# Kernel tuning notes

Hardware: AMD Instinct MI355X
Metric: run time of the kernel (lower is better)

## Reference

```python
import jax, jax.numpy as jnp
import numpy as np


def _rope_tables(T, d):
    half = d // 2
    i = jnp.arange(half, dtype=jnp.float32)
    theta = 10000.0 ** (-2.0 * i / d)          # [half]
    m = jnp.arange(T, dtype=jnp.float32)[:, None]  # [T,1]
    ang = m * theta[None, :]                    # [T,half]
    return jnp.cos(ang), jnp.sin(ang)


def _rotate(v, cos, sin):
    # interleaved even/odd RoPE rotation, vectorized
    B, T, d = v.shape
    half = d // 2
    v2 = v.reshape(B, T, half, 2)
    even, odd = v2[..., 0], v2[..., 1]
    c = cos[None, :, :]
    s = sin[None, :, :]
    new_even = even * c - odd * s
    new_odd = even * s + odd * c
    return jnp.stack([new_even, new_odd], axis=-1).reshape(B, T, d)


def setup_inputs() -> dict:
    key = jax.random.key(0)
    k1, k2, k3, k4 = jax.random.split(key, 4)
    B, T, d = 4, 2048, 1024
    x = jax.random.normal(k1, (B, T, d), dtype=jnp.float32)
    scale = 0.02
    Wq = jax.random.normal(k2, (d, d), dtype=jnp.float32) * scale
    Wk = jax.random.normal(k3, (d, d), dtype=jnp.float32) * scale
    Wv = jax.random.normal(k4, (d, d), dtype=jnp.float32) * scale
    return {"x": x, "Wq": Wq, "Wk": Wk, "Wv": Wv}


def reference(x, Wq, Wk, Wv):
    B, T, d = x.shape
    cos, sin = _rope_tables(T, d)
    # torch Linear: y = x @ W.T
    Q = jnp.einsum('btd,ed->bte', x, Wq)
    K = jnp.einsum('btd,ed->bte', x, Wk)
    V = jnp.einsum('btd,ed->bte', x, Wv)
    Qr = _rotate(Q, cos, sin)
    Kr = _rotate(K, cos, sin)
    scores = jnp.einsum('bqd,bkd->bqk', Qr, Kr) / jnp.sqrt(jnp.float32(d))
    # NOTE: original uses tril with diagonal=1 (allows one future position)
    mask = jnp.tril(jnp.ones((T, T), dtype=bool), k=1)
    scores = jnp.where(mask[None, :, :], scores, -jnp.inf)
    attn = jax.nn.softmax(scores, axis=-1)
    out = jnp.einsum('bqk,bkd->bqd', attn, V)
    return out
```

## Files before the change

kernel.cpp:

```cpp
#include <hip/hip_runtime.h>


typedef float f32x4 __attribute__((ext_vector_type(4)));
typedef __bf16 bf16x8 __attribute__((ext_vector_type(8)));

#define BM 128
#define BN 128
#define BK 64

#define SP_BATCH 2473984

__device__ __forceinline__ unsigned short f2bf(float f) {
  union { float f; unsigned int u; } c; c.f = f;
  unsigned int u = c.u;
  u += 0x7fffu + ((u >> 16) & 1u);
  return (unsigned short)(u >> 16);
}
__device__ __forceinline__ float bf2f(unsigned short h) {
  union { unsigned int u; float f; } c; c.u = ((unsigned int)h) << 16;
  return c.f;
}

__device__ __forceinline__ void async16(const unsigned short* gp, unsigned short* lp) {
  __builtin_amdgcn_global_load_lds(
      (const __attribute__((address_space(1))) void*)gp,
      (__attribute__((address_space(3))) void*)lp, 16, 0, 0);
}

__global__ __launch_bounds__(256) void cvt_all(
    const float4* __restrict__ x, const float4* __restrict__ wq,
    const float4* __restrict__ wk, const float4* __restrict__ wv,
    ushort4* __restrict__ xb, ushort4* __restrict__ wb,
    float4* __restrict__ rowsums) {
  int b = blockIdx.x, t = threadIdx.x;
  if (b == 11264) {
#pragma unroll
    for (int i = 0; i < 8; ++i) rowsums[i * 256 + t] = float4{0.f, 0.f, 0.f, 0.f};
    return;
  }
  const float4* src;
  ushort4* dst;
  long i;
  if (b < 8192) { src = x; dst = xb; i = (long)b * 256 + t; }
  else if (b < 9216) { src = wq; dst = wb; i = (long)(b - 8192) * 256 + t; }
  else if (b < 10240) { src = wk; dst = wb + 262144; i = (long)(b - 9216) * 256 + t; }
  else { src = wv; dst = wb + 524288; i = (long)(b - 10240) * 256 + t; }
  float4 v = src[i];
  ushort4 o;
  o.x = f2bf(v.x); o.y = f2bf(v.y); o.z = f2bf(v.z); o.w = f2bf(v.w);
  dst[i] = o;
}

template <int IM, int JN>
__device__ __forceinline__ void gemm_body(
    const unsigned short* __restrict__ A, const unsigned short* __restrict__ B,
    unsigned short* As, unsigned short* Bs,
    int lda, int ldb, int m0, int n0, int ktiles,
    int tid, int lane, int wave, f32x4 (&acc)[IM][JN]) {
  const int wm = (wave >> 1) * (IM * 16);
  const int wn = (wave & 1) * (JN * 16);
  const int fm = lane & 15;
  const int q = lane >> 4;
  const int srow = tid >> 3;
  const int c = (tid & 7) ^ (srow & 7);
  const unsigned short* Ab = A + (long)(m0 + srow) * lda + c * 8;
  const unsigned short* Bb = B + (long)(n0 + srow) * ldb + c * 8;
  unsigned short* ldA = As + tid * 8;
  unsigned short* ldB = Bs + tid * 8;

  for (int kt = 0; kt < ktiles; ++kt) {
    const long k0 = (long)kt * BK;
    __syncthreads();
#pragma unroll
    for (int p = 0; p < IM; ++p)
      async16(Ab + (long)(p * 32) * lda + k0, ldA + p * 2048);
#pragma unroll
    for (int p = 0; p < JN; ++p)
      async16(Bb + (long)(p * 32) * ldb + k0, ldB + p * 2048);
    __syncthreads();

#pragma unroll
    for (int s = 0; s < 2; ++s) {
      bf16x8 af[IM], bfr[JN];
#pragma unroll
      for (int i = 0; i < IM; ++i) {
        int row = wm + i * 16 + fm;
        af[i] = *(const bf16x8*)&As[row * 64 + ((((s << 2) | q) ^ (row & 7)) << 3)];
      }
#pragma unroll
      for (int j = 0; j < JN; ++j) {
        int row = wn + j * 16 + fm;
        bfr[j] = *(const bf16x8*)&Bs[row * 64 + ((((s << 2) | q) ^ (row & 7)) << 3)];
      }
#pragma unroll
      for (int i = 0; i < IM; ++i)
#pragma unroll
        for (int j = 0; j < JN; ++j)
          acc[i][j] = __builtin_amdgcn_mfma_f32_16x16x32_bf16(af[i], bfr[j], acc[i][j], 0, 0, 0);
    }
  }
}

__global__ __launch_bounds__(256, 4) void qkv_rope_gemm(
    const unsigned short* __restrict__ A, const unsigned short* __restrict__ B,
    unsigned short* __restrict__ Qr, unsigned short* __restrict__ Kr,
    unsigned short* __restrict__ Vt) {
  __shared__ __align__(16) unsigned short As[BM * BK];
  __shared__ __align__(16) unsigned short Bs[BN * BK];
  const int tid = threadIdx.x, lane = tid & 63, wave = tid >> 6;
  const int bm = blockIdx.x, bn = blockIdx.y;
  const int m0 = bm * BM, n0 = bn * BN;
  const int wm = (wave >> 1) * 64, wn = (wave & 1) * 64;
  const int q = lane >> 4, fm = lane & 15;

  f32x4 acc[4][4];
#pragma unroll
  for (int i = 0; i < 4; ++i)
#pragma unroll
    for (int j = 0; j < 4; ++j) acc[i][j] = (f32x4)(0.f);

  gemm_body<4, 4>(A, B, As, Bs, 1024, 1024, m0, n0, 16, tid, lane, wave, acc);

  if (n0 < 2048) {
    const float NEG = -13.287712379549449f / 1024.f;
    unsigned short* dst = (n0 < 1024) ? Qr : Kr;
    const int t00 = (m0 + wm + q * 4) & 2047;
#pragma unroll
    for (int j = 0; j < 4; ++j) {
      int c = (n0 & 1023) + wn + j * 16 + fm;
      float th = exp2f((float)(c & ~1) * NEG);
      float sgn = (c & 1) ? 1.f : -1.f;
      float ang0 = (float)t00 * th;
      float cb = __cosf(ang0), sb = __sinf(ang0);
      float c1 = __cosf(th), s1 = __sinf(th);
      float c16 = __cosf(16.f * th), s16 = __sinf(16.f * th);
#pragma unroll
      for (int i = 0; i < 4; ++i) {
        int gmB = m0 + wm + i * 16 + q * 4;
        float cr = cb, sr = sb;
#pragma unroll
        for (int r = 0; r < 4; ++r) {
          float v = acc[i][j][r];
          float p = __shfl_xor(v, 1);
          dst[(long)(gmB + r) * 1024 + c] = f2bf(v * cr + sgn * p * sr);
          float crn = cr * c1 - sr * s1;
          sr = sr * c1 + cr * s1;
          cr = crn;
        }
        float cbn = cb * c16 - sb * s16;
        sb = sb * c16 + cb * s16;
        cb = cbn;
      }
    }
  } else {
    const int c0 = n0 - 2048;
#pragma unroll
    for (int j = 0; j < 4; ++j) {
      int c = c0 + wn + j * 16 + fm;
#pragma unroll
      for (int i = 0; i < 4; ++i) {
        int gmB = m0 + wm + i * 16 + q * 4;
        int b = gmB >> 11, t = gmB & 2047;
        ushort4 pk;
        pk.x = f2bf(acc[i][j][0]);
        pk.y = f2bf(acc[i][j][1]);
        pk.z = f2bf(acc[i][j][2]);
        pk.w = f2bf(acc[i][j][3]);
        *(ushort4*)&Vt[((long)b * 1024 + c) * 2048 + t] = pk;
      }
    }
  }
}

__global__ __launch_bounds__(256, 4) void s_gemm(
    const unsigned short* __restrict__ Qr, const unsigned short* __restrict__ Kr,
    unsigned short* __restrict__ Sp, float* __restrict__ rowsums) {
  __shared__ __align__(16) unsigned short As[64 * BK];
  __shared__ __align__(16) unsigned short Bs[BN * BK];
  const int tid = threadIdx.x, lane = tid & 63, wave = tid >> 6;
  const int z = blockIdx.z;
  int idx = blockIdx.x, b = 31;
#pragma unroll 1
  for (; b > 0; --b) {
    int cnt = ((b >> 1) + 2 > 16) ? 16 : (b >> 1) + 2;
    if (idx < cnt) break;
    idx -= cnt;
  }
  const int bn = idx;
  const int sb = b >> 1;
  const int len = ((sb + 2 > 16) ? 16 : sb + 2) * 128;
  unsigned short* S = Sp + (long)z * SP_BATCH + (long)(sb * (sb + 3) / 2) * 16384 +
                      (long)(b & 1) * 64 * len;

  if (128 * bn > 64 * b + 64) {
    ushort4 zz{0, 0, 0, 0};
#pragma unroll
    for (int u = 0; u < 8; ++u) {
      int e = tid * 8 + u;
      int row = e >> 5, c4 = e & 31;
      *(ushort4*)&S[(long)row * len + bn * 128 + c4 * 4] = zz;
    }
    return;
  }

  const unsigned short* A = Qr + (long)z * 2048 * 1024;
  const unsigned short* B = Kr + (long)z * 2048 * 1024;
  float* rs = rowsums + (long)z * 2048;
  const int m0 = b * 64, n0 = bn * 128;
  const int wm = (wave >> 1) * 32, wn = (wave & 1) * 64;
  const int q = lane >> 4, fm = lane & 15;

  f32x4 acc[2][4];
#pragma unroll
  for (int i = 0; i < 2; ++i)
#pragma unroll
    for (int j = 0; j < 4; ++j) acc[i][j] = (f32x4)(0.f);

  gemm_body<2, 4>(A, B, As, Bs, 1024, 1024, m0, n0, 16, tid, lane, wave, acc);

  float* rsum = (float*)Bs;
  __syncthreads();
  if (tid < 64) rsum[tid] = 0.f;
  __syncthreads();

#pragma unroll
  for (int i = 0; i < 2; ++i) {
    int lr = wm + i * 16 + q * 4;
    int gmB = m0 + lr;
    float ps[4] = {0.f, 0.f, 0.f, 0.f};
#pragma unroll
    for (int j = 0; j < 4; ++j) {
      int gn = n0 + wn + j * 16 + fm;
#pragma unroll
      for (int r = 0; r < 4; ++r) {
        float e = (gn <= gmB + r + 1) ? __expf(acc[i][j][r] * 0.03125f) : 0.f;
        unsigned short h = f2bf(e);
        S[(long)(lr + r) * len + gn] = h;
        ps[r] += bf2f(h);
      }
    }
#pragma unroll
    for (int r = 0; r < 4; ++r) {
      float v = ps[r];
      v += __shfl_xor(v, 1);
      v += __shfl_xor(v, 2);
      v += __shfl_xor(v, 4);
      v += __shfl_xor(v, 8);
      if (fm == 0) atomicAdd(&rsum[lr + r], v);
    }
  }
  __syncthreads();
  if (tid < 64) atomicAdd(&rs[m0 + tid], rsum[tid]);
}

__global__ __launch_bounds__(256, 4) void pv_gemm(
    const unsigned short* __restrict__ Sp, const unsigned short* __restrict__ Vt,
    const float* __restrict__ rowsums, float* __restrict__ out) {
  __shared__ __align__(16) unsigned short As[64 * BK];
  __shared__ __align__(16) unsigned short Bs[128 * BK];
  const int tid = threadIdx.x, lane = tid & 63, wave = tid >> 6;
  const int bn = blockIdx.x & 7;
  const int z = blockIdx.x >> 3;
  const int bm = 31 - blockIdx.y;
  const int sb = bm >> 1;
  const int lda = ((sb + 2 > 16) ? 16 : sb + 2) * 128;
  const unsigned short* A = Sp + (long)z * SP_BATCH +
                            (long)(sb * (sb + 3) / 2) * 16384 +
                            (long)(bm & 1) * 64 * lda;
  const unsigned short* B = Vt + (long)z * 1024 * 2048;
  const float* rs = rowsums + (long)z * 2048;
  float* C = out + (long)z * 2048 * 1024;
  int ktiles = bm + 2;
  if (ktiles > 32) ktiles = 32;
  const int m0 = bm * 64, n0 = bn * 128;
  const int wm = (wave >> 1) * 32, wn = (wave & 1) * 64;
  const int q = lane >> 4, fm = lane & 15;

  f32x4 acc[2][4];
#pragma unroll
  for (int i = 0; i < 2; ++i)
#pragma unroll
    for (int j = 0; j < 4; ++j) acc[i][j] = (f32x4)(0.f);

  gemm_body<2, 4>(A, B, As, Bs, lda, 2048, 0, n0, ktiles, tid, lane, wave, acc);

#pragma unroll
  for (int i = 0; i < 2; ++i) {
    int gmB = m0 + wm + i * 16 + q * 4;
#pragma unroll
    for (int r = 0; r < 4; ++r) {
      float inv = 1.f / rs[gmB + r];
#pragma unroll
      for (int j = 0; j < 4; ++j) {
        int gn = n0 + wn + j * 16 + fm;
        C[(long)(gmB + r) * 1024 + gn] = acc[i][j][r] * inv;
      }
    }
  }
}

extern "C" void kernel_launch(void* const* d_in, const int* in_sizes, int n_in,
                              void* d_out, int out_size, void* d_ws, size_t ws_size,
                              hipStream_t stream) {
  const float* x = (const float*)d_in[0];
  const float* Wq = (const float*)d_in[1];
  const float* Wk = (const float*)d_in[2];
  const float* Wv = (const float*)d_in[3];
  float* out = (float*)d_out;

  float* rowsums = (float*)d_ws;
  unsigned short* Qr = (unsigned short*)d_ws + 16384;
  unsigned short* Kr = Qr + (long)8192 * 1024;
  unsigned short* Vt = Kr + (long)8192 * 1024;
  unsigned short* xb = Vt + (long)8192 * 1024;
  unsigned short* Wb = xb + (long)8192 * 1024;

  cvt_all<<<11265, 256, 0, stream>>>((const float4*)x, (const float4*)Wq,
                                     (const float4*)Wk, (const float4*)Wv,
                                     (ushort4*)xb, (ushort4*)Wb, (float4*)rowsums);

  qkv_rope_gemm<<<dim3(64, 24), 256, 0, stream>>>(xb, Wb, Qr, Kr, Vt);

  unsigned short* Sp = xb;
  s_gemm<<<dim3(302, 1, 4), 256, 0, stream>>>(Qr, Kr, Sp, rowsums);
  pv_gemm<<<dim3(32, 32), 256, 0, stream>>>(Sp, Vt, rowsums, out);
}
```

Baseline: 219.2 us.

## Split QKV GEMM into 256x256 QK-RoPE kernel with 4-stage pipeline and separate V GEMM

Replaces the single fused QKV projection kernel with two launches. A new 512-thread kernel computes Q and K on 256x256 tiles using a 4-deep async LDS ring buffer (BK=32), explicit vmcnt waits and raised MFMA priority, then applies RoPE in its epilogue. V is produced by the old 128x128 kernel in a separate launch with a transposed store. The larger tile gives more reuse per load, at the cost of an extra launch, fewer blocks for the QK part (256 blocks), and an unswizzled LDS layout that may cause bank conflicts.

```diff
diff --git a/kernel.cpp b/kernel.cpp
--- a/kernel.cpp
+++ b/kernel.cpp
@@ -101,9 +101,114 @@
   }
 }
 
-__global__ __launch_bounds__(256, 4) void qkv_rope_gemm(
+__global__ __launch_bounds__(512, 2) void qk_rope_gemm256(
     const unsigned short* __restrict__ A, const unsigned short* __restrict__ B,
-    unsigned short* __restrict__ Qr, unsigned short* __restrict__ Kr,
+    unsigned short* __restrict__ Qr, unsigned short* __restrict__ Kr) {
+  __shared__ __align__(16) unsigned short lds[4][2][8192];
+  const int tid = threadIdx.x, lane = tid & 63, wave = tid >> 6;
+  const int m0 = blockIdx.x * 256, n0 = blockIdx.y * 256;
+  const int wm = (wave >> 2) * 128, wn = (wave & 3) * 64;
+  const int q = lane >> 4, fm = lane & 15;
+  const int r0 = tid >> 2, c16 = tid & 3;
+
+  const unsigned short* Ab = A + (long)(m0 + r0) * 1024 + c16 * 8;
+  const unsigned short* Bb = B + (long)(n0 + r0) * 1024 + c16 * 8;
+
+  f32x4 acc[8][4];
+#pragma unroll
+  for (int i = 0; i < 8; ++i)
+#pragma unroll
+    for (int j = 0; j < 4; ++j) acc[i][j] = (f32x4)(0.f);
+
+#define QSTAGE(kt)                                                     \
+  {                                                                    \
+    const int bi_ = (kt) & 3;                                          \
+    const int ko_ = (kt) * 32;                                         \
+    async16(Ab + ko_, &lds[bi_][0][tid * 8]);                          \
+    async16(Ab + 131072 + ko_, &lds[bi_][0][tid * 8 + 4096]);          \
+    async16(Bb + ko_, &lds[bi_][1][tid * 8]);                          \
+    async16(Bb + 131072 + ko_, &lds[bi_][1][tid * 8 + 4096]);          \
+  }
+
+#define QCOMPUTE(kt)                                                   \
+  {                                                                    \
+    const int bi_ = (kt) & 3;                                          \
+    const unsigned short* As_ = lds[bi_][0];                           \
+    const unsigned short* Bs_ = lds[bi_][1];                           \
+    bf16x8 af[8], bfr[4];                                              \
+    _Pragma("unroll") for (int i = 0; i < 8; ++i)                      \
+        af[i] = *(const bf16x8*)&As_[((wm + i * 16 + fm) * 4 + q) * 8];\
+    _Pragma("unroll") for (int j = 0; j < 4; ++j)                      \
+        bfr[j] = *(const bf16x8*)&Bs_[((wn + j * 16 + fm) * 4 + q) * 8];\
+    __builtin_amdgcn_s_setprio(1);                                     \
+    _Pragma("unroll") for (int i = 0; i < 8; ++i)                      \
+        _Pragma("unroll") for (int j = 0; j < 4; ++j)                  \
+            acc[i][j] = __builtin_amdgcn_mfma_f32_16x16x32_bf16(       \
+                af[i], bfr[j], acc[i][j], 0, 0, 0);                    \
+    __builtin_amdgcn_s_setprio(0);                                     \
+  }
+
+  QSTAGE(0); QSTAGE(1); QSTAGE(2);
+#pragma unroll 1
+  for (int kt = 0; kt < 29; ++kt) {
+    QSTAGE(kt + 3);
+    asm volatile("s_waitcnt vmcnt(12)" ::: "memory");
+    __builtin_amdgcn_s_barrier();
+    __builtin_amdgcn_sched_barrier(0);
+    QCOMPUTE(kt);
+    __builtin_amdgcn_s_barrier();
+  }
+  asm volatile("s_waitcnt vmcnt(8)" ::: "memory");
+  __builtin_amdgcn_s_barrier();
+  __builtin_amdgcn_sched_barrier(0);
+  QCOMPUTE(29);
+  __builtin_amdgcn_s_barrier();
+  asm volatile("s_waitcnt vmcnt(4)" ::: "memory");
+  __builtin_amdgcn_s_barrier();
+  __builtin_amdgcn_sched_barrier(0);
+  QCOMPUTE(30);
+  __builtin_amdgcn_s_barrier();
+  asm volatile("s_waitcnt vmcnt(0)" ::: "memory");
+  __builtin_amdgcn_s_barrier();
+  __builtin_amdgcn_sched_barrier(0);
+  QCOMPUTE(31);
+
+  const float NEG = -13.287712379549449f / 1024.f;
+  unsigned short* dst = (n0 < 1024) ? Qr : Kr;
+  const int t00 = (m0 + wm + q * 4) & 2047;
+#pragma unroll
+  for (int j = 0; j < 4; ++j) {
+    int c = (n0 & 1023) + wn + j * 16 + fm;
+    float th = exp2f((float)(c & ~1) * NEG);
+    float sgn = (c & 1) ? 1.f : -1.f;
+    float ang0 = (float)t00 * th;
+    float cb = __cosf(ang0), sb = __sinf(ang0);
+    float c1 = __cosf(th), s1 = __sinf(th);
+    float cst = __cosf(16.f * th), sst = __sinf(16.f * th);
+#pragma unroll
+    for (int i = 0; i < 8; ++i) {
+      int gmB = m0 + wm + i * 16 + q * 4;
+      float cr = cb, sr = sb;
+#pragma unroll
+      for (int r = 0; r < 4; ++r) {
+        float v = acc[i][j][r];
+        float p = __shfl_xor(v, 1);
+        dst[(long)(gmB + r) * 1024 + c] = f2bf(v * cr + sgn * p * sr);
+        float crn = cr * c1 - sr * s1;
+        sr = sr * c1 + cr * s1;
+        cr = crn;
+      }
+      float cbn = cb * cst - sb * sst;
+      sb = sb * cst + cb * sst;
+      cb = cbn;
+    }
+  }
+#undef QSTAGE
+#undef QCOMPUTE
+}
+
+__global__ __launch_bounds__(256, 4) void v_gemm(
+    const unsigned short* __restrict__ A, const unsigned short* __restrict__ B,
     unsigned short* __restrict__ Vt) {
   __shared__ __align__(16) unsigned short As[BM * BK];
   __shared__ __align__(16) unsigned short Bs[BN * BK];
@@ -121,53 +226,19 @@
 
   gemm_body<4, 4>(A, B, As, Bs, 1024, 1024, m0, n0, 16, tid, lane, wave, acc);
 
-  if (n0 < 2048) {
-    const float NEG = -13.287712379549449f / 1024.f;
-    unsigned short* dst = (n0 < 1024) ? Qr : Kr;
-    const int t00 = (m0 + wm + q * 4) & 2047;
-#pragma unroll
-    for (int j = 0; j < 4; ++j) {
-      int c = (n0 & 1023) + wn + j * 16 + fm;
-      float th = exp2f((float)(c & ~1) * NEG);
-      float sgn = (c & 1) ? 1.f : -1.f;
-      float ang0 = (float)t00 * th;
-      float cb = __cosf(ang0), sb = __sinf(ang0);
-      float c1 = __cosf(th), s1 = __sinf(th);
-      float c16 = __cosf(16.f * th), s16 = __sinf(16.f * th);
-#pragma unroll
-      for (int i = 0; i < 4; ++i) {
-        int gmB = m0 + wm + i * 16 + q * 4;
-        float cr = cb, sr = sb;
-#pragma unroll
-        for (int r = 0; r < 4; ++r) {
-          float v = acc[i][j][r];
-          float p = __shfl_xor(v, 1);
-          dst[(long)(gmB + r) * 1024 + c] = f2bf(v * cr + sgn * p * sr);
-          float crn = cr * c1 - sr * s1;
-          sr = sr * c1 + cr * s1;
-          cr = crn;
-        }
-        float cbn = cb * c16 - sb * s16;
-        sb = sb * c16 + cb * s16;
-        cb = cbn;
-      }
-    }
-  } else {
-    const int c0 = n0 - 2048;
-#pragma unroll
-    for (int j = 0; j < 4; ++j) {
-      int c = c0 + wn + j * 16 + fm;
-#pragma unroll
-      for (int i = 0; i < 4; ++i) {
-        int gmB = m0 + wm + i * 16 + q * 4;
-        int b = gmB >> 11, t = gmB & 2047;
-        ushort4 pk;
-        pk.x = f2bf(acc[i][j][0]);
-        pk.y = f2bf(acc[i][j][1]);
-        pk.z = f2bf(acc[i][j][2]);
-        pk.w = f2bf(acc[i][j][3]);
-        *(ushort4*)&Vt[((long)b * 1024 + c) * 2048 + t] = pk;
-      }
+#pragma unroll
+  for (int j = 0; j < 4; ++j) {
+    int c = n0 + wn + j * 16 + fm;
+#pragma unroll
+    for (int i = 0; i < 4; ++i) {
+      int gmB = m0 + wm + i * 16 + q * 4;
+      int b = gmB >> 11, t = gmB & 2047;
+      ushort4 pk;
+      pk.x = f2bf(acc[i][j][0]);
+      pk.y = f2bf(acc[i][j][1]);
+      pk.z = f2bf(acc[i][j][2]);
+      pk.w = f2bf(acc[i][j][3]);
+      *(ushort4*)&Vt[((long)b * 1024 + c) * 2048 + t] = pk;
     }
   }
 }
@@ -319,7 +390,8 @@
                                      (const float4*)Wk, (const float4*)Wv,
                                      (ushort4*)xb, (ushort4*)Wb, (float4*)rowsums);
 
-  qkv_rope_gemm<<<dim3(64, 24), 256, 0, stream>>>(xb, Wb, Qr, Kr, Vt);
+  qk_rope_gemm256<<<dim3(32, 8), 512, 0, stream>>>(xb, Wb, Qr, Kr);
+  v_gemm<<<dim3(64, 8), 256, 0, stream>>>(xb, Wb + (long)2048 * 1024, Vt);
 
   unsigned short* Sp = xb;
   s_gemm<<<dim3(302, 1, 4), 256, 0, stream>>>(Qr, Kr, Sp, rowsums);
```

Measured after the change: 232.6 us. 1.06x slower.
